# Kernel tuning notes

Hardware: AMD Instinct MI355X
Metric: run time of the kernel (lower is better)

## Reference

```python
import jax, jax.numpy as jnp
import numpy as np

B, C, T, K = 16, 512, 2048, 64

def setup_inputs() -> dict:
    key = jax.random.key(0)
    k1, k2, k3 = jax.random.split(key, 3)
    v = jax.random.normal(k1, (B, C, T), dtype=jnp.float32)
    # 1x1 Conv1d weights == linear maps over channel dim
    Wk = jax.random.normal(k2, (K, C), dtype=jnp.float32) * 0.02
    bk = jnp.zeros((K,), dtype=jnp.float32)
    Wq = jax.random.normal(k3, (K, C), dtype=jnp.float32) * 0.02
    bq = jnp.zeros((K,), dtype=jnp.float32)
    gamma = jnp.ones((), dtype=jnp.float32)
    return {"v": v, "Wk": Wk, "bk": bk, "Wq": Wq, "bq": bq, "gamma": gamma}

def reference(v, Wk, bk, Wq, bq, gamma):
    # k, q: (B, K, T) via 1x1 conv = channel-wise linear
    k = jnp.einsum('kc,bct->bkt', Wk, v) + bk[None, :, None]
    q = jnp.einsum('kc,bct->bkt', Wq, v) + bq[None, :, None]
    # original: e1[b,d,i,j]=q[b,d,j], e2[b,d,i,j]=k[b,d,i]; sum over d
    # -> s[b,i,j] = sum_d k[b,d,i] * q[b,d,j]  (avoid materializing B,K,T,T)
    s = jnp.einsum('bdi,bdj->bij', k, q)  # (B, T, T)
    a = jax.nn.softmax(s, axis=1)          # softmax over dim=1 (the i axis)
    att = jnp.einsum('bct,btj->bcj', v, a)  # bmm(v, a)
    return v + gamma * att
```

## Files before the change

kernel.cpp:

```cpp
#include <hip/hip_runtime.h>

#define Bc 16
#define Cc 512
#define Tc 2048
#define QT 128
#define KT 64
#define PST 72
#define LTS 66
#define EPS 132

typedef __attribute__((ext_vector_type(8))) short short8;
typedef __attribute__((ext_vector_type(4))) float f32x4;
typedef unsigned short u16;

static __device__ __forceinline__ u16 f2bf(float x) {
  unsigned u = __float_as_uint(x);
  u += 0x7FFF + ((u >> 16) & 1);
  return (u16)(u >> 16);
}

static __device__ __forceinline__ unsigned cvt_pk_bf16(float lo, float hi) {
  unsigned r;
  asm("v_cvt_pk_bf16_f32 %0, %1, %2" : "=v"(r) : "v"(lo), "v"(hi));
  return r;
}

static __device__ __forceinline__ void block_sync_lds() {
  __builtin_amdgcn_sched_barrier(0);
  asm volatile("s_waitcnt lgkmcnt(0)" ::: "memory");
  __builtin_amdgcn_s_barrier();
  __builtin_amdgcn_sched_barrier(0);
}

__global__ __launch_bounds__(256) void prep_kernel(
    const float* __restrict__ Wk, const float* __restrict__ Wq,
    const float* __restrict__ bk, const float* __restrict__ bq,
    u16* __restrict__ Wbf, float* __restrict__ bkq)
{
  int idx  = blockIdx.x * 256 + threadIdx.x;
  int base = idx * 4;
  if (base < 128 * Cc) {
    int ch = base >> 9;
    int c  = base & (Cc - 1);
    const float* src = (ch < 64) ? (Wk + (size_t)ch * Cc + c)
                                 : (Wq + (size_t)(ch - 64) * Cc + c);
    f32x4 w = *reinterpret_cast<const f32x4*>(src);
    uint2 o;
    o.x = (unsigned)f2bf(w[0]) | ((unsigned)f2bf(w[1]) << 16);
    o.y = (unsigned)f2bf(w[2]) | ((unsigned)f2bf(w[3]) << 16);
    *reinterpret_cast<uint2*>(Wbf + base) = o;
  }
  if (idx < 128) bkq[idx] = (idx < 64) ? bk[idx] : bq[idx - 64];
}

__global__ __launch_bounds__(256) void kqv_kernel(
    const float* __restrict__ v, const u16* __restrict__ Wbf,
    const float* __restrict__ bkq, u16* __restrict__ kq, u16* __restrict__ vbf)
{
  __shared__ u16 LDSt[2][64][LTS];
  const int b   = blockIdx.y;
  const int t0  = blockIdx.x * 64;
  const int tid = threadIdx.x;
  const int lane = tid & 63;
  const int w    = tid >> 6;
  const int l15  = lane & 15;
  const int lg   = lane >> 4;

  f32x4 acc[8];
  #pragma unroll
  for (int mt = 0; mt < 8; ++mt) acc[mt] = f32x4{0.f, 0.f, 0.f, 0.f};

  const float* vb = v + (size_t)b * Cc * Tc + t0;
  float x[16];
  #pragma unroll
  for (int r = 0; r < 16; ++r) x[r] = vb[(size_t)(w * 16 + r) * Tc + lane];

  int buf = 0;
  for (int c0 = 0; c0 < Cc; c0 += 64, buf ^= 1) {
    #pragma unroll
    for (int r = 0; r < 16; ++r) {
      u16 hb = f2bf(x[r]);
      LDSt[buf][lane][w * 16 + r] = hb;
      vbf[((size_t)b * Cc + c0 + w * 16 + r) * Tc + t0 + lane] = hb;
    }
    block_sync_lds();
    if (c0 + 64 < Cc) {
      #pragma unroll
      for (int r = 0; r < 16; ++r)
        x[r] = vb[(size_t)(c0 + 64 + w * 16 + r) * Tc + lane];
    }
    #pragma unroll
    for (int ks = 0; ks < 2; ++ks) {
      short8 bfrag = *reinterpret_cast<const short8*>(&LDSt[buf][w * 16 + l15][ks * 32 + lg * 8]);
      #pragma unroll
      for (int mt = 0; mt < 8; ++mt) {
        short8 afrag = *reinterpret_cast<const short8*>(
            Wbf + (size_t)(mt * 16 + l15) * Cc + c0 + ks * 32 + lg * 8);
        acc[mt] = __builtin_amdgcn_mfma_f32_16x16x32_bf16(afrag, bfrag, acc[mt], 0, 0, 0);
      }
    }
  }
  const int t = t0 + w * 16 + l15;
  u16* op = kq + ((size_t)b * Tc + t) * 128;
  #pragma unroll
  for (int mt = 0; mt < 8; ++mt) {
    int chb = mt * 16 + lg * 4;
    uint2 o;
    o.x = cvt_pk_bf16(acc[mt][0] + bkq[chb + 0], acc[mt][1] + bkq[chb + 1]);
    o.y = cvt_pk_bf16(acc[mt][2] + bkq[chb + 2], acc[mt][3] + bkq[chb + 3]);
    *reinterpret_cast<uint2*>(op + chb) = o;
  }
}

__global__ __launch_bounds__(512, 2) void attn_kernel(
    const float* __restrict__ v, const u16* __restrict__ vbf,
    const u16* __restrict__ kq, const float* __restrict__ gamma_p,
    float* __restrict__ out)
{
  __shared__ u16 P[2][QT * PST];
  __shared__ float lsum_lds[QT];
  __shared__ float linv_lds[QT];

  const int L   = blockIdx.x;
  const int lin = (L & 7) * 32 + (L >> 3);
  const int b   = lin >> 4;
  const int j0  = (lin & 15) * QT;
  const int tid = threadIdx.x;
  const int lane = tid & 63;
  const int wid  = tid >> 6;
  const int l15  = lane & 15;
  const int lg   = lane >> 4;
  const int c0   = wid * 64;

  short8 qf0, qf1;
  {
    const u16* qp = kq + (size_t)(b * Tc + j0 + wid * 16 + l15) * 128 + 64 + lg * 8;
    qf0 = *reinterpret_cast<const short8*>(qp);
    qf1 = *reinterpret_cast<const short8*>(qp + 32);
  }

  f32x4 O[4][8];
  #pragma unroll
  for (int a = 0; a < 4; ++a)
    #pragma unroll
    for (int bb = 0; bb < 8; ++bb) O[a][bb] = f32x4{0.f, 0.f, 0.f, 0.f};

  float lsum = 0.f;

  const u16* kbase = kq + (size_t)b * Tc * 128 + lg * 8;
  const u16* vbase = vbf + ((size_t)b * Cc + c0) * Tc;

  short8 kf[4][2];
  short8 vf0[4];

  #pragma unroll
  for (int it = 0; it < 4; ++it) {
    const u16* kp = kbase + (size_t)(it * 16 + l15) * 128;
    kf[it][0] = *reinterpret_cast<const short8*>(kp);
    kf[it][1] = *reinterpret_cast<const short8*>(kp + 32);
  }
  #pragma unroll
  for (int ct = 0; ct < 4; ++ct)
    vf0[ct] = *reinterpret_cast<const short8*>(
        vbase + (size_t)(ct * 16 + l15) * Tc + lg * 8);
  {
    f32x4 sacc[4];
    #pragma unroll
    for (int it = 0; it < 4; ++it) {
      f32x4 s = f32x4{0.f, 0.f, 0.f, 0.f};
      s = __builtin_amdgcn_mfma_f32_16x16x32_bf16(kf[it][0], qf0, s, 0, 0, 0);
      s = __builtin_amdgcn_mfma_f32_16x16x32_bf16(kf[it][1], qf1, s, 0, 0, 0);
      sacc[it] = s;
    }
    u16* prow = &P[0][(wid * 16 + l15) * PST];
    #pragma unroll
    for (int it = 0; it < 4; ++it) {
      float p0 = __expf(sacc[it][0]);
      float p1 = __expf(sacc[it][1]);
      float p2 = __expf(sacc[it][2]);
      float p3 = __expf(sacc[it][3]);
      lsum += (p0 + p1) + (p2 + p3);
      uint2 wv;
      wv.x = cvt_pk_bf16(p0, p1);
      wv.y = cvt_pk_bf16(p2, p3);
      *reinterpret_cast<uint2*>(prow + it * 16 + lg * 4) = wv;
    }
  }
  #pragma unroll
  for (int it = 0; it < 4; ++it) {
    const u16* kp = kbase + (size_t)(KT + it * 16 + l15) * 128;
    kf[it][0] = *reinterpret_cast<const short8*>(kp);
    kf[it][1] = *reinterpret_cast<const short8*>(kp + 32);
  }
  block_sync_lds();

  int pb = 0;
  for (int i0 = 0; i0 < Tc; i0 += KT, pb ^= 1) {
    const bool last = (i0 + KT >= Tc);

    short8 vf1[4];
    #pragma unroll
    for (int ct = 0; ct < 4; ++ct)
      vf1[ct] = *reinterpret_cast<const short8*>(
          vbase + (size_t)(ct * 16 + l15) * Tc + i0 + 32 + lg * 8);

    if (!last) {
      f32x4 sacc[4];
      #pragma unroll
      for (int it = 0; it < 4; ++it) {
        f32x4 s = f32x4{0.f, 0.f, 0.f, 0.f};
        s = __builtin_amdgcn_mfma_f32_16x16x32_bf16(kf[it][0], qf0, s, 0, 0, 0);
        s = __builtin_amdgcn_mfma_f32_16x16x32_bf16(kf[it][1], qf1, s, 0, 0, 0);
        sacc[it] = s;
      }
      u16* prow = &P[pb ^ 1][(wid * 16 + l15) * PST];
      #pragma unroll
      for (int it = 0; it < 4; ++it) {
        float p0 = __expf(sacc[it][0]);
        float p1 = __expf(sacc[it][1]);
        float p2 = __expf(sacc[it][2]);
        float p3 = __expf(sacc[it][3]);
        lsum += (p0 + p1) + (p2 + p3);
        uint2 wv;
        wv.x = cvt_pk_bf16(p0, p1);
        wv.y = cvt_pk_bf16(p2, p3);
        *reinterpret_cast<uint2*>(prow + it * 16 + lg * 4) = wv;
      }
    }

    __builtin_amdgcn_s_setprio(1);
    {
      short8 pf[8];
      #pragma unroll
      for (int jj = 0; jj < 8; ++jj)
        pf[jj] = *reinterpret_cast<const short8*>(
            &P[pb][(jj * 16 + l15) * PST + lg * 8]);
      #pragma unroll
      for (int ct = 0; ct < 4; ++ct)
        #pragma unroll
        for (int jj = 0; jj < 8; ++jj)
          O[ct][jj] = __builtin_amdgcn_mfma_f32_16x16x32_bf16(vf0[ct], pf[jj], O[ct][jj], 0, 0, 0);
    }
    {
      short8 pf[8];
      #pragma unroll
      for (int jj = 0; jj < 8; ++jj)
        pf[jj] = *reinterpret_cast<const short8*>(
            &P[pb][(jj * 16 + l15) * PST + 32 + lg * 8]);
      #pragma unroll
      for (int ct = 0; ct < 4; ++ct)
        #pragma unroll
        for (int jj = 0; jj < 8; ++jj)
          O[ct][jj] = __builtin_amdgcn_mfma_f32_16x16x32_bf16(vf1[ct], pf[jj], O[ct][jj], 0, 0, 0);
    }
    __builtin_amdgcn_s_setprio(0);

    if (!last) {
      if (i0 + 2 * KT < Tc) {
        #pragma unroll
        for (int it = 0; it < 4; ++it) {
          const u16* kp = kbase + (size_t)(i0 + 2 * KT + it * 16 + l15) * 128;
          kf[it][0] = *reinterpret_cast<const short8*>(kp);
          kf[it][1] = *reinterpret_cast<const short8*>(kp + 32);
        }
      }
      #pragma unroll
      for (int ct = 0; ct < 4; ++ct)
        vf0[ct] = *reinterpret_cast<const short8*>(
            vbase + (size_t)(ct * 16 + l15) * Tc + (i0 + KT) + lg * 8);
      block_sync_lds();
    }
  }

  lsum += __shfl_xor(lsum, 16);
  lsum += __shfl_xor(lsum, 32);
  if (lane < 16) lsum_lds[wid * 16 + lane] = lsum;
  __syncthreads();
  const float gamma = *gamma_p;
  if (tid < QT) linv_lds[tid] = gamma / lsum_lds[tid];
  __syncthreads();

  float* ep = reinterpret_cast<float*>(&P[0][0]) + wid * (8 * EPS);
  const int half_sel = lg >> 1;
  const int cl_base  = (lg & 1) * 4;
  const int rd_cl = lane & 7;
  const int rd_jq = lane >> 3;

  #pragma unroll
  for (int r = 0; r < 8; ++r) {
    const int ct = r >> 1;
    const int hs = r & 1;
    if (half_sel == hs) {
      #pragma unroll
      for (int jj = 0; jj < 8; ++jj) {
        #pragma unroll
        for (int rr = 0; rr < 4; ++rr)
          ep[(cl_base + rr) * EPS + jj * 16 + l15] = O[ct][jj][rr];
      }
    }
    asm volatile("s_waitcnt lgkmcnt(0)" ::: "memory");
    __builtin_amdgcn_sched_barrier(0);
    const int c_glob = c0 + ct * 16 + hs * 8 + rd_cl;
    const float* vrow = v + ((size_t)(b * Cc + c_glob)) * Tc + j0;
    float* orow = out + ((size_t)(b * Cc + c_glob)) * Tc + j0;
    #pragma unroll
    for (int q = 0; q < 4; ++q) {
      const int jf = (rd_jq + 8 * q) * 4;
      f32x4 o4 = *reinterpret_cast<const f32x4*>(&ep[rd_cl * EPS + jf]);
      f32x4 li = *reinterpret_cast<const f32x4*>(&linv_lds[jf]);
      f32x4 v4 = *reinterpret_cast<const f32x4*>(&vrow[jf]);
      f32x4 o;
      o[0] = v4[0] + li[0] * o4[0];
      o[1] = v4[1] + li[1] * o4[1];
      o[2] = v4[2] + li[2] * o4[2];
      o[3] = v4[3] + li[3] * o4[3];
      *reinterpret_cast<f32x4*>(&orow[jf]) = o;
    }
    asm volatile("s_waitcnt lgkmcnt(0)" ::: "memory");
    __builtin_amdgcn_sched_barrier(0);
  }
}

extern "C" void kernel_launch(void* const* d_in, const int* in_sizes, int n_in,
                              void* d_out, int out_size, void* d_ws, size_t ws_size,
                              hipStream_t stream) {
  const float* v  = (const float*)d_in[0];
  const float* Wk = (const float*)d_in[1];
  const float* bk = (const float*)d_in[2];
  const float* Wq = (const float*)d_in[3];
  const float* bq = (const float*)d_in[4];
  const float* gm = (const float*)d_in[5];
  float* out = (float*)d_out;

  char* ws = (char*)d_ws;
  u16*   kqb = (u16*)ws;
  u16*   vbf = (u16*)(ws + 8388608);
  u16*   Wbf = (u16*)(ws + 8388608 + 33554432);
  float* bkq = (float*)(ws + 8388608 + 33554432 + 131072);

  prep_kernel<<<dim3(64), dim3(256), 0, stream>>>(Wk, Wq, bk, bq, Wbf, bkq);
  kqv_kernel<<<dim3(Tc / 64, Bc), dim3(256), 0, stream>>>(v, Wbf, bkq, kqb, vbf);
  attn_kernel<<<dim3((Tc / QT) * Bc), dim3(512), 0, stream>>>(v, vbf, kqb, gm, out);
}
```

Measured before the change: 191.5 us.

## Double key-tile size to 128 and restructure score/PV pipeline per iteration

Raises the key tile from 64 to 128 rows, so each iteration computes two 64-row score blocks into one LDS buffer and then runs four PV MFMA chunks with ping-ponged V fragments. This halves the number of block barriers and reorders the K and V global loads so they are prefetched between MFMA groups. It also drops the s_setprio hints and changes the epilogue lane mapping, so that each group of 8 lanes covers one channel row across 32 contiguous float4 columns. The score computation is no longer overlapped with the previous tile's PV work, which may expose exp and latency, and LDS use per block grows.

```diff
diff --git a/kernel.cpp b/kernel.cpp
--- a/kernel.cpp
+++ b/kernel.cpp
@@ -4,8 +4,8 @@
 #define Cc 512
 #define Tc 2048
 #define QT 128
-#define KT 64
-#define PST 72
+#define KT 128
+#define PST2 136
 #define LTS 66
 #define EPS 132
 
@@ -117,9 +117,9 @@
     const u16* __restrict__ kq, const float* __restrict__ gamma_p,
     float* __restrict__ out)
 {
-  __shared__ u16 P[2][QT * PST];
+  __shared__ u16 P[2][QT * PST2];
   __shared__ float lsum_lds[QT];
-  __shared__ float linv_lds[QT];
+  __shared__ __align__(16) float linv_lds[QT];
 
   const int L   = blockIdx.x;
   const int lin = (L & 7) * 32 + (L >> 3);
@@ -151,7 +151,7 @@
   const u16* vbase = vbf + ((size_t)b * Cc + c0) * Tc;
 
   short8 kf[4][2];
-  short8 vf0[4];
+  short8 vfA[4], vfB[4];
 
   #pragma unroll
   for (int it = 0; it < 4; ++it) {
@@ -161,9 +161,14 @@
   }
   #pragma unroll
   for (int ct = 0; ct < 4; ++ct)
-    vf0[ct] = *reinterpret_cast<const short8*>(
+    vfA[ct] = *reinterpret_cast<const short8*>(
         vbase + (size_t)(ct * 16 + l15) * Tc + lg * 8);
-  {
+
+  int pb = 0;
+  for (int i0 = 0; i0 < Tc; i0 += KT, pb ^= 1) {
+    const bool last = (i0 + KT >= Tc);
+    u16* prow = &P[pb][(wid * 16 + l15) * PST2];
+
     f32x4 sacc[4];
     #pragma unroll
     for (int it = 0; it < 4; ++it) {
@@ -172,7 +177,12 @@
       s = __builtin_amdgcn_mfma_f32_16x16x32_bf16(kf[it][1], qf1, s, 0, 0, 0);
       sacc[it] = s;
     }
-    u16* prow = &P[0][(wid * 16 + l15) * PST];
+    #pragma unroll
+    for (int it = 0; it < 4; ++it) {
+      const u16* kp = kbase + (size_t)(i0 + 64 + it * 16 + l15) * 128;
+      kf[it][0] = *reinterpret_cast<const short8*>(kp);
+      kf[it][1] = *reinterpret_cast<const short8*>(kp + 32);
+    }
     #pragma unroll
     for (int it = 0; it < 4; ++it) {
       float p0 = __expf(sacc[it][0]);
@@ -185,90 +195,102 @@
       wv.y = cvt_pk_bf16(p2, p3);
       *reinterpret_cast<uint2*>(prow + it * 16 + lg * 4) = wv;
     }
-  }
-  #pragma unroll
-  for (int it = 0; it < 4; ++it) {
-    const u16* kp = kbase + (size_t)(KT + it * 16 + l15) * 128;
-    kf[it][0] = *reinterpret_cast<const short8*>(kp);
-    kf[it][1] = *reinterpret_cast<const short8*>(kp + 32);
-  }
-  block_sync_lds();
-
-  int pb = 0;
-  for (int i0 = 0; i0 < Tc; i0 += KT, pb ^= 1) {
-    const bool last = (i0 + KT >= Tc);
-
-    short8 vf1[4];
+
+    #pragma unroll
+    for (int it = 0; it < 4; ++it) {
+      f32x4 s = f32x4{0.f, 0.f, 0.f, 0.f};
+      s = __builtin_amdgcn_mfma_f32_16x16x32_bf16(kf[it][0], qf0, s, 0, 0, 0);
+      s = __builtin_amdgcn_mfma_f32_16x16x32_bf16(kf[it][1], qf1, s, 0, 0, 0);
+      sacc[it] = s;
+    }
+    if (!last) {
+      #pragma unroll
+      for (int it = 0; it < 4; ++it) {
+        const u16* kp = kbase + (size_t)(i0 + KT + it * 16 + l15) * 128;
+        kf[it][0] = *reinterpret_cast<const short8*>(kp);
+        kf[it][1] = *reinterpret_cast<const short8*>(kp + 32);
+      }
+    }
+    #pragma unroll
+    for (int it = 0; it < 4; ++it) {
+      float p0 = __expf(sacc[it][0]);
+      float p1 = __expf(sacc[it][1]);
+      float p2 = __expf(sacc[it][2]);
+      float p3 = __expf(sacc[it][3]);
+      lsum += (p0 + p1) + (p2 + p3);
+      uint2 wv;
+      wv.x = cvt_pk_bf16(p0, p1);
+      wv.y = cvt_pk_bf16(p2, p3);
+      *reinterpret_cast<uint2*>(prow + 64 + it * 16 + lg * 4) = wv;
+    }
+
+    block_sync_lds();
+
     #pragma unroll
     for (int ct = 0; ct < 4; ++ct)
-      vf1[ct] = *reinterpret_cast<const short8*>(
+      vfB[ct] = *reinterpret_cast<const short8*>(
           vbase + (size_t)(ct * 16 + l15) * Tc + i0 + 32 + lg * 8);
-
-    if (!last) {
-      f32x4 sacc[4];
-      #pragma unroll
-      for (int it = 0; it < 4; ++it) {
-        f32x4 s = f32x4{0.f, 0.f, 0.f, 0.f};
-        s = __builtin_amdgcn_mfma_f32_16x16x32_bf16(kf[it][0], qf0, s, 0, 0, 0);
-        s = __builtin_amdgcn_mfma_f32_16x16x32_bf16(kf[it][1], qf1, s, 0, 0, 0);
-        sacc[it] = s;
-      }
-      u16* prow = &P[pb ^ 1][(wid * 16 + l15) * PST];
-      #pragma unroll
-      for (int it = 0; it < 4; ++it) {
-        float p0 = __expf(sacc[it][0]);
-        float p1 = __expf(sacc[it][1]);
-        float p2 = __expf(sacc[it][2]);
-        float p3 = __expf(sacc[it][3]);
-        lsum += (p0 + p1) + (p2 + p3);
-        uint2 wv;
-        wv.x = cvt_pk_bf16(p0, p1);
-        wv.y = cvt_pk_bf16(p2, p3);
-        *reinterpret_cast<uint2*>(prow + it * 16 + lg * 4) = wv;
-      }
-    }
-
-    __builtin_amdgcn_s_setprio(1);
     {
       short8 pf[8];
       #pragma unroll
       for (int jj = 0; jj < 8; ++jj)
         pf[jj] = *reinterpret_cast<const short8*>(
-            &P[pb][(jj * 16 + l15) * PST + lg * 8]);
+            &P[pb][(jj * 16 + l15) * PST2 + lg * 8]);
       #pragma unroll
       for (int ct = 0; ct < 4; ++ct)
         #pragma unroll
         for (int jj = 0; jj < 8; ++jj)
-          O[ct][jj] = __builtin_amdgcn_mfma_f32_16x16x32_bf16(vf0[ct], pf[jj], O[ct][jj], 0, 0, 0);
-    }
+          O[ct][jj] = __builtin_amdgcn_mfma_f32_16x16x32_bf16(vfA[ct], pf[jj], O[ct][jj], 0, 0, 0);
+    }
+    #pragma unroll
+    for (int ct = 0; ct < 4; ++ct)
+      vfA[ct] = *reinterpret_cast<const short8*>(
+          vbase + (size_t)(ct * 16 + l15) * Tc + i0 + 64 + lg * 8);
     {
       short8 pf[8];
       #pragma unroll
       for (int jj = 0; jj < 8; ++jj)
         pf[jj] = *reinterpret_cast<const short8*>(
-            &P[pb][(jj * 16 + l15) * PST + 32 + lg * 8]);
+            &P[pb][(jj * 16 + l15) * PST2 + 32 + lg * 8]);
       #pragma unroll
       for (int ct = 0; ct < 4; ++ct)
         #pragma unroll
         for (int jj = 0; jj < 8; ++jj)
-          O[ct][jj] = __builtin_amdgcn_mfma_f32_16x16x32_bf16(vf1[ct], pf[jj], O[ct][jj], 0, 0, 0);
-    }
-    __builtin_amdgcn_s_setprio(0);
-
+          O[ct][jj] = __builtin_amdgcn_mfma_f32_16x16x32_bf16(vfB[ct], pf[jj], O[ct][jj], 0, 0, 0);
+    }
+    #pragma unroll
+    for (int ct = 0; ct < 4; ++ct)
+      vfB[ct] = *reinterpret_cast<const short8*>(
+          vbase + (size_t)(ct * 16 + l15) * Tc + i0 + 96 + lg * 8);
+    {
+      short8 pf[8];
+      #pragma unroll
+      for (int jj = 0; jj < 8; ++jj)
+        pf[jj] = *reinterpret_cast<const short8*>(
+            &P[pb][(jj * 16 + l15) * PST2 + 64 + lg * 8]);
+      #pragma unroll
+      for (int ct = 0; ct < 4; ++ct)
+        #pragma unroll
+        for (int jj = 0; jj < 8; ++jj)
+          O[ct][jj] = __builtin_amdgcn_mfma_f32_16x16x32_bf16(vfA[ct], pf[jj], O[ct][jj], 0, 0, 0);
+    }
     if (!last) {
-      if (i0 + 2 * KT < Tc) {
-        #pragma unroll
-        for (int it = 0; it < 4; ++it) {
-          const u16* kp = kbase + (size_t)(i0 + 2 * KT + it * 16 + l15) * 128;
-          kf[it][0] = *reinterpret_cast<const short8*>(kp);
-          kf[it][1] = *reinterpret_cast<const short8*>(kp + 32);
-        }
-      }
-      #pragma unroll
-      for (int ct = 0; ct < 4; ++ct)
-        vf0[ct] = *reinterpret_cast<const short8*>(
-            vbase + (size_t)(ct * 16 + l15) * Tc + (i0 + KT) + lg * 8);
-      block_sync_lds();
+      #pragma unroll
+      for (int ct = 0; ct < 4; ++ct)
+        vfA[ct] = *reinterpret_cast<const short8*>(
+            vbase + (size_t)(ct * 16 + l15) * Tc + i0 + KT + lg * 8);
+    }
+    {
+      short8 pf[8];
+      #pragma unroll
+      for (int jj = 0; jj < 8; ++jj)
+        pf[jj] = *reinterpret_cast<const short8*>(
+            &P[pb][(jj * 16 + l15) * PST2 + 96 + lg * 8]);
+      #pragma unroll
+      for (int ct = 0; ct < 4; ++ct)
+        #pragma unroll
+        for (int jj = 0; jj < 8; ++jj)
+          O[ct][jj] = __builtin_amdgcn_mfma_f32_16x16x32_bf16(vfB[ct], pf[jj], O[ct][jj], 0, 0, 0);
     }
   }
 
@@ -283,8 +305,8 @@
   float* ep = reinterpret_cast<float*>(&P[0][0]) + wid * (8 * EPS);
   const int half_sel = lg >> 1;
   const int cl_base  = (lg & 1) * 4;
-  const int rd_cl = lane & 7;
-  const int rd_jq = lane >> 3;
+  const int rd_rw = lane >> 3;
+  const int rd_ch = lane & 7;
 
   #pragma unroll
   for (int r = 0; r < 8; ++r) {
@@ -292,21 +314,20 @@
     const int hs = r & 1;
     if (half_sel == hs) {
       #pragma unroll
-      for (int jj = 0; jj < 8; ++jj) {
+      for (int jj = 0; jj < 8; ++jj)
         #pragma unroll
         for (int rr = 0; rr < 4; ++rr)
           ep[(cl_base + rr) * EPS + jj * 16 + l15] = O[ct][jj][rr];
-      }
     }
     asm volatile("s_waitcnt lgkmcnt(0)" ::: "memory");
     __builtin_amdgcn_sched_barrier(0);
-    const int c_glob = c0 + ct * 16 + hs * 8 + rd_cl;
+    const int c_glob = c0 + ct * 16 + hs * 8 + rd_rw;
     const float* vrow = v + ((size_t)(b * Cc + c_glob)) * Tc + j0;
     float* orow = out + ((size_t)(b * Cc + c_glob)) * Tc + j0;
     #pragma unroll
-    for (int q = 0; q < 4; ++q) {
-      const int jf = (rd_jq + 8 * q) * 4;
-      f32x4 o4 = *reinterpret_cast<const f32x4*>(&ep[rd_cl * EPS + jf]);
+    for (int qq = 0; qq < 4; ++qq) {
+      const int jf = (rd_ch + 8 * qq) * 4;
+      f32x4 o4 = *reinterpret_cast<const f32x4*>(&ep[rd_rw * EPS + jf]);
       f32x4 li = *reinterpret_cast<const f32x4*>(&linv_lds[jf]);
       f32x4 v4 = *reinterpret_cast<const f32x4*>(&vrow[jf]);
       f32x4 o;
```

Result: slower. 315.3 us (+64.6%).
